# Performance work log

Hardware: AMD Instinct MI355X
Metric: run time of the kernel (lower is better)

The kernel has to match this reference:

```python
import jax, jax.numpy as jnp
import numpy as np

N_NODES = 20000
N_EDGES = 640000
IN_F = 128
CL1_F = 128
CL2_F = 128
OUT_F = 2


def setup_inputs() -> dict:
    key = jax.random.key(0)
    ks = jax.random.split(key, 8)
    x = jax.random.normal(ks[0], (N_NODES, IN_F), dtype=jnp.float32)
    edge_index = jax.random.randint(ks[1], (2, N_EDGES), 0, N_NODES, dtype=jnp.int64)
    s1 = 1.0 / np.sqrt(IN_F)
    s2 = 1.0 / np.sqrt(CL1_F)
    s3 = 1.0 / np.sqrt(CL2_F)
    W1 = jax.random.uniform(ks[2], (IN_F, CL1_F), jnp.float32, -s1, s1)
    b1 = jax.random.uniform(ks[3], (CL1_F,), jnp.float32, -s1, s1)
    W2 = jax.random.uniform(ks[4], (CL1_F, CL2_F), jnp.float32, -s2, s2)
    b2 = jax.random.uniform(ks[5], (CL2_F,), jnp.float32, -s2, s2)
    W3 = jax.random.uniform(ks[6], (CL2_F, OUT_F), jnp.float32, -s3, s3)
    b3 = jax.random.uniform(ks[7], (OUT_F,), jnp.float32, -s3, s3)
    return {"x": x, "edge_index": edge_index, "W1": W1, "b1": b1,
            "W2": W2, "b2": b2, "W3": W3, "b3": b3}


def _scatter_mean(feat_src, src, dst, n_nodes):
    # out[i] = mean over edges e with dst[e]==i of feat_src gathered at src[e]
    msg = feat_src[src]                                   # [E, F] gather
    summed = jax.ops.segment_sum(msg, dst, num_segments=n_nodes)  # [N, F]
    ones = jnp.ones((src.shape[0],), dtype=feat_src.dtype)
    cnt = jax.ops.segment_sum(ones, dst, num_segments=n_nodes)    # [N]
    return summed / jnp.maximum(cnt, 1.0)[:, None]


def _mpnn_layer(x, src, dst, W, b, n_nodes):
    aggr = _scatter_mean(x, src, dst, n_nodes)
    return jax.nn.relu(aggr @ W + b)


def reference(x, edge_index, W1, b1, W2, b2, W3, b3):
    src, dst = edge_index[0], edge_index[1]
    n = x.shape[0]
    h = _mpnn_layer(x, src, dst, W1, b1, n)   # conv1 (update relu); extra relu is no-op
    h = _mpnn_layer(h, src, dst, W2, b2, n)   # conv2
    # dropout in eval mode is identity
    return h @ W3 + b3
```

## Files before the change

### kernel.cpp

```cpp
#include <hip/hip_runtime.h>

#define N_NODES 20000
#define N_EDGES 640000
#define F 128
#define CAP 128


__global__ __launch_bounds__(256)
void bucket_kernel(const int* __restrict__ src, const int* __restrict__ dst,
                   int* __restrict__ cnt, int* __restrict__ bucket) {
    int e = blockIdx.x * blockDim.x + threadIdx.x;
    if (e >= N_EDGES) return;
    int d = dst[e];
    int pos = atomicAdd(&cnt[d], 1);
    if (pos < CAP) bucket[(size_t)d * CAP + pos] = src[e];
}

__global__ __launch_bounds__(256)
void gemm_kernel(const float* __restrict__ A, const float* __restrict__ W,
                 float* __restrict__ C) {
    __shared__ float As[32][F + 4];
    int tid  = threadIdx.x;
    int row0 = blockIdx.x * 32;

    const float4* A4 = (const float4*)(A + (size_t)row0 * F);
    for (int i = tid; i < 32 * 32; i += 256) {
        float4 v = A4[i];
        int r = i >> 5, c4 = (i & 31) * 4;
        *(float4*)&As[r][c4] = v;
    }
    __syncthreads();

    int tx = tid & 31, ty = tid >> 5;
    int c0 = tx * 4, r0 = ty * 4;
    float acc[4][4] = {};

    for (int k = 0; k < F; k += 4) {
        float4 a4[4];
#pragma unroll
        for (int i = 0; i < 4; ++i) a4[i] = *(const float4*)&As[r0 + i][k];
#pragma unroll
        for (int u = 0; u < 4; ++u) {
            float4 w = *(const float4*)(W + (size_t)(k + u) * F + c0);
#pragma unroll
            for (int i = 0; i < 4; ++i) {
                float a = (u == 0) ? a4[i].x : (u == 1) ? a4[i].y : (u == 2) ? a4[i].z : a4[i].w;
                acc[i][0] += a * w.x;
                acc[i][1] += a * w.y;
                acc[i][2] += a * w.z;
                acc[i][3] += a * w.w;
            }
        }
    }

#pragma unroll
    for (int i = 0; i < 4; ++i) {
        float4 o;
        o.x = acc[i][0]; o.y = acc[i][1]; o.z = acc[i][2]; o.w = acc[i][3];
        *(float4*)(C + (size_t)(row0 + r0 + i) * F + c0) = o;
    }
}

__global__ __launch_bounds__(256)
void agg_bias_relu_kernel(const float* __restrict__ y, const int* __restrict__ cnt,
                          const int* __restrict__ bucket, const float* __restrict__ b,
                          float* __restrict__ out) {
    int wid  = (blockIdx.x * blockDim.x + threadIdx.x) >> 6;
    int lane = threadIdx.x & 63;
    if (wid >= N_NODES) return;
    int half = lane >> 5;
    int sub  = lane & 31;
    int deg  = cnt[wid];
    const int* lst = bucket + (size_t)wid * CAP;
    const float4* f4 = (const float4*)y;

    float4 acc; acc.x = acc.y = acc.z = acc.w = 0.f;
    int j = 0;
    for (; j + 16 <= deg; j += 16) {
        int4 ia = *(const int4*)(lst + j);
        int4 ib = *(const int4*)(lst + j + 4);
        int4 ic = *(const int4*)(lst + j + 8);
        int4 id = *(const int4*)(lst + j + 12);
        int i0 = half ? ia.y : ia.x;
        int i1 = half ? ia.w : ia.z;
        int i2 = half ? ib.y : ib.x;
        int i3 = half ? ib.w : ib.z;
        int i4 = half ? ic.y : ic.x;
        int i5 = half ? ic.w : ic.z;
        int i6 = half ? id.y : id.x;
        int i7 = half ? id.w : id.z;
        float4 v0 = f4[(size_t)i0 * 32 + sub];
        float4 v1 = f4[(size_t)i1 * 32 + sub];
        float4 v2 = f4[(size_t)i2 * 32 + sub];
        float4 v3 = f4[(size_t)i3 * 32 + sub];
        float4 v4 = f4[(size_t)i4 * 32 + sub];
        float4 v5 = f4[(size_t)i5 * 32 + sub];
        float4 v6 = f4[(size_t)i6 * 32 + sub];
        float4 v7 = f4[(size_t)i7 * 32 + sub];
        acc.x += ((v0.x + v1.x) + (v2.x + v3.x)) + ((v4.x + v5.x) + (v6.x + v7.x));
        acc.y += ((v0.y + v1.y) + (v2.y + v3.y)) + ((v4.y + v5.y) + (v6.y + v7.y));
        acc.z += ((v0.z + v1.z) + (v2.z + v3.z)) + ((v4.z + v5.z) + (v6.z + v7.z));
        acc.w += ((v0.w + v1.w) + (v2.w + v3.w)) + ((v4.w + v5.w) + (v6.w + v7.w));
    }
    for (; j + 2 <= deg; j += 2) {
        int2 ii = *(const int2*)(lst + j);
        int idx = half ? ii.y : ii.x;
        float4 v = f4[(size_t)idx * 32 + sub];
        acc.x += v.x; acc.y += v.y; acc.z += v.z; acc.w += v.w;
    }
    if (j < deg && half == 0) {
        float4 v = f4[(size_t)lst[j] * 32 + sub];
        acc.x += v.x; acc.y += v.y; acc.z += v.z; acc.w += v.w;
    }
    acc.x += __shfl(acc.x, lane ^ 32);
    acc.y += __shfl(acc.y, lane ^ 32);
    acc.z += __shfl(acc.z, lane ^ 32);
    acc.w += __shfl(acc.w, lane ^ 32);

    if (half == 0) {
        float inv = 1.0f / fmaxf((float)deg, 1.0f);
        float4 bv = ((const float4*)b)[sub];
        float4 o;
        o.x = fmaxf(acc.x * inv + bv.x, 0.f);
        o.y = fmaxf(acc.y * inv + bv.y, 0.f);
        o.z = fmaxf(acc.z * inv + bv.z, 0.f);
        o.w = fmaxf(acc.w * inv + bv.w, 0.f);
        ((float4*)out)[(size_t)wid * 32 + sub] = o;
    }
}

__global__ __launch_bounds__(256)
void agg_final_kernel(const float* __restrict__ y, const int* __restrict__ cnt,
                      const int* __restrict__ bucket, const float* __restrict__ b,
                      const float* __restrict__ W3, const float* __restrict__ b3,
                      float* __restrict__ out) {
    int wid  = (blockIdx.x * blockDim.x + threadIdx.x) >> 6;
    int lane = threadIdx.x & 63;
    if (wid >= N_NODES) return;
    int half = lane >> 5;
    int sub  = lane & 31;
    int deg  = cnt[wid];
    const int* lst = bucket + (size_t)wid * CAP;
    const float4* f4 = (const float4*)y;

    float4 acc; acc.x = acc.y = acc.z = acc.w = 0.f;
    int j = 0;
    for (; j + 16 <= deg; j += 16) {
        int4 ia = *(const int4*)(lst + j);
        int4 ib = *(const int4*)(lst + j + 4);
        int4 ic = *(const int4*)(lst + j + 8);
        int4 id = *(const int4*)(lst + j + 12);
        int i0 = half ? ia.y : ia.x;
        int i1 = half ? ia.w : ia.z;
        int i2 = half ? ib.y : ib.x;
        int i3 = half ? ib.w : ib.z;
        int i4 = half ? ic.y : ic.x;
        int i5 = half ? ic.w : ic.z;
        int i6 = half ? id.y : id.x;
        int i7 = half ? id.w : id.z;
        float4 v0 = f4[(size_t)i0 * 32 + sub];
        float4 v1 = f4[(size_t)i1 * 32 + sub];
        float4 v2 = f4[(size_t)i2 * 32 + sub];
        float4 v3 = f4[(size_t)i3 * 32 + sub];
        float4 v4 = f4[(size_t)i4 * 32 + sub];
        float4 v5 = f4[(size_t)i5 * 32 + sub];
        float4 v6 = f4[(size_t)i6 * 32 + sub];
        float4 v7 = f4[(size_t)i7 * 32 + sub];
        acc.x += ((v0.x + v1.x) + (v2.x + v3.x)) + ((v4.x + v5.x) + (v6.x + v7.x));
        acc.y += ((v0.y + v1.y) + (v2.y + v3.y)) + ((v4.y + v5.y) + (v6.y + v7.y));
        acc.z += ((v0.z + v1.z) + (v2.z + v3.z)) + ((v4.z + v5.z) + (v6.z + v7.z));
        acc.w += ((v0.w + v1.w) + (v2.w + v3.w)) + ((v4.w + v5.w) + (v6.w + v7.w));
    }
    for (; j + 2 <= deg; j += 2) {
        int2 ii = *(const int2*)(lst + j);
        int idx = half ? ii.y : ii.x;
        float4 v = f4[(size_t)idx * 32 + sub];
        acc.x += v.x; acc.y += v.y; acc.z += v.z; acc.w += v.w;
    }
    if (j < deg && half == 0) {
        float4 v = f4[(size_t)lst[j] * 32 + sub];
        acc.x += v.x; acc.y += v.y; acc.z += v.z; acc.w += v.w;
    }
    acc.x += __shfl(acc.x, lane ^ 32);
    acc.y += __shfl(acc.y, lane ^ 32);
    acc.z += __shfl(acc.z, lane ^ 32);
    acc.w += __shfl(acc.w, lane ^ 32);

    float inv = 1.0f / fmaxf((float)deg, 1.0f);
    float4 bv = ((const float4*)b)[sub];
    float h0 = fmaxf(acc.x * inv + bv.x, 0.f);
    float h1 = fmaxf(acc.y * inv + bv.y, 0.f);
    float h2 = fmaxf(acc.z * inv + bv.z, 0.f);
    float h3 = fmaxf(acc.w * inv + bv.w, 0.f);
    float2 w0 = ((const float2*)W3)[sub * 4];
    float2 w1 = ((const float2*)W3)[sub * 4 + 1];
    float2 w2 = ((const float2*)W3)[sub * 4 + 2];
    float2 w3 = ((const float2*)W3)[sub * 4 + 3];
    float p0 = h0 * w0.x + h1 * w1.x + h2 * w2.x + h3 * w3.x;
    float p1 = h0 * w0.y + h1 * w1.y + h2 * w2.y + h3 * w3.y;
#pragma unroll
    for (int off = 16; off > 0; off >>= 1) {
        p0 += __shfl_down(p0, off, 32);
        p1 += __shfl_down(p1, off, 32);
    }
    if (lane == 0) {
        float2 o; o.x = p0 + b3[0]; o.y = p1 + b3[1];
        *(float2*)(out + (size_t)wid * 2) = o;
    }
}

extern "C" void kernel_launch(void* const* d_in, const int* in_sizes, int n_in,
                              void* d_out, int out_size, void* d_ws, size_t ws_size,
                              hipStream_t stream) {
    const float* x   = (const float*)d_in[0];
    const int*   ei  = (const int*)d_in[1];
    const int*   src = ei;
    const int*   dst = ei + N_EDGES;
    const float* W1 = (const float*)d_in[2];
    const float* b1 = (const float*)d_in[3];
    const float* W2 = (const float*)d_in[4];
    const float* b2 = (const float*)d_in[5];
    const float* W3 = (const float*)d_in[6];
    const float* b3 = (const float*)d_in[7];
    float* out = (float*)d_out;

    char* base = (char*)d_ws;
    size_t off = 0;
    auto take = [&](size_t bytes) -> char* {
        char* p = base + off;
        off += (bytes + 255) & ~(size_t)255;
        return p;
    };
    int*   cnt    = (int*)  take(N_NODES * sizeof(int));
    int*   bucket = (int*)  take((size_t)N_NODES * CAP * sizeof(int));
    float* y      = (float*)take((size_t)N_NODES * F * sizeof(float));
    float* h      = (float*)take((size_t)N_NODES * F * sizeof(float));

    hipMemsetAsync(cnt, 0, N_NODES * sizeof(int), stream);
    bucket_kernel<<<(N_EDGES + 255) / 256, 256, 0, stream>>>(src, dst, cnt, bucket);

    gemm_kernel<<<N_NODES / 32, 256, 0, stream>>>(x, W1, y);
    agg_bias_relu_kernel<<<(N_NODES * 64) / 256, 256, 0, stream>>>(y, cnt, bucket, b1, h);
    gemm_kernel<<<N_NODES / 32, 256, 0, stream>>>(h, W2, y);
    agg_final_kernel<<<(N_NODES * 64) / 256, 256, 0, stream>>>(y, cnt, bucket, b2, W3, b3, out);
}
```

Measured before the change: 215.2 us.

## Fuse edge bucketing into first GEMM launch and split aggregation across two waves

Merges the edge-bucketing kernel into the first GEMM launch by appending extra blocks that do the atomic bucket fill, so the two independent stages share one launch and can overlap. The aggregation kernels now give each node two waves that split the 16-neighbor chunks between them and combine their partial sums through shared memory. This doubles the parallelism per node to hide gather latency, at the cost of a block-wide barrier, shared-memory traffic, and half of the waves sitting idle during the epilogue.

```diff
diff --git a/kernel.cpp b/kernel.cpp
--- a/kernel.cpp
+++ b/kernel.cpp
@@ -4,25 +4,85 @@
 #define N_EDGES 640000
 #define F 128
 #define CAP 128
-
-
-__global__ __launch_bounds__(256)
-void bucket_kernel(const int* __restrict__ src, const int* __restrict__ dst,
-                   int* __restrict__ cnt, int* __restrict__ bucket) {
-    int e = blockIdx.x * blockDim.x + threadIdx.x;
-    if (e >= N_EDGES) return;
-    int d = dst[e];
-    int pos = atomicAdd(&cnt[d], 1);
-    if (pos < CAP) bucket[(size_t)d * CAP + pos] = src[e];
-}
-
-__global__ __launch_bounds__(256)
-void gemm_kernel(const float* __restrict__ A, const float* __restrict__ W,
-                 float* __restrict__ C) {
+#define GEMM_BLOCKS (N_NODES / 32)
+#define BUCKET_BLOCKS (N_EDGES / 256)
+
+
+__device__ __forceinline__ void gather16(const float4* __restrict__ f4,
+                                         const int* __restrict__ lst, int j,
+                                         int half, int sub, float4& acc) {
+    int4 ia = *(const int4*)(lst + j);
+    int4 ib = *(const int4*)(lst + j + 4);
+    int4 ic = *(const int4*)(lst + j + 8);
+    int4 id = *(const int4*)(lst + j + 12);
+    int i0 = half ? ia.y : ia.x;
+    int i1 = half ? ia.w : ia.z;
+    int i2 = half ? ib.y : ib.x;
+    int i3 = half ? ib.w : ib.z;
+    int i4 = half ? ic.y : ic.x;
+    int i5 = half ? ic.w : ic.z;
+    int i6 = half ? id.y : id.x;
+    int i7 = half ? id.w : id.z;
+    float4 v0 = f4[(size_t)i0 * 32 + sub];
+    float4 v1 = f4[(size_t)i1 * 32 + sub];
+    float4 v2 = f4[(size_t)i2 * 32 + sub];
+    float4 v3 = f4[(size_t)i3 * 32 + sub];
+    float4 v4 = f4[(size_t)i4 * 32 + sub];
+    float4 v5 = f4[(size_t)i5 * 32 + sub];
+    float4 v6 = f4[(size_t)i6 * 32 + sub];
+    float4 v7 = f4[(size_t)i7 * 32 + sub];
+    acc.x += ((v0.x + v1.x) + (v2.x + v3.x)) + ((v4.x + v5.x) + (v6.x + v7.x));
+    acc.y += ((v0.y + v1.y) + (v2.y + v3.y)) + ((v4.y + v5.y) + (v6.y + v7.y));
+    acc.z += ((v0.z + v1.z) + (v2.z + v3.z)) + ((v4.z + v5.z) + (v6.z + v7.z));
+    acc.w += ((v0.w + v1.w) + (v2.w + v3.w)) + ((v4.w + v5.w) + (v6.w + v7.w));
+}
+
+__device__ __forceinline__ float4 wave_gather(const float4* __restrict__ f4,
+                                              const int* __restrict__ lst, int deg,
+                                              int wh, int half, int sub, int lane) {
+    float4 acc; acc.x = acc.y = acc.z = acc.w = 0.f;
+    int nfull = deg >> 4;
+    for (int c = wh; c < nfull; c += 2)
+        gather16(f4, lst, c << 4, half, sub, acc);
+    if (wh == (nfull & 1)) {
+        int j = nfull << 4;
+        for (; j + 2 <= deg; j += 2) {
+            int2 ii = *(const int2*)(lst + j);
+            int idx = half ? ii.y : ii.x;
+            float4 v = f4[(size_t)idx * 32 + sub];
+            acc.x += v.x; acc.y += v.y; acc.z += v.z; acc.w += v.w;
+        }
+        if (j < deg && half == 0) {
+            float4 v = f4[(size_t)lst[j] * 32 + sub];
+            acc.x += v.x; acc.y += v.y; acc.z += v.z; acc.w += v.w;
+        }
+    }
+    acc.x += __shfl(acc.x, lane ^ 32);
+    acc.y += __shfl(acc.y, lane ^ 32);
+    acc.z += __shfl(acc.z, lane ^ 32);
+    acc.w += __shfl(acc.w, lane ^ 32);
+    return acc;
+}
+
+__global__ __launch_bounds__(256)
+void gemm_bucket_kernel(const float* __restrict__ A, const float* __restrict__ W,
+                        float* __restrict__ C,
+                        const int* __restrict__ src, const int* __restrict__ dst,
+                        int* __restrict__ cnt, int* __restrict__ bucket) {
     __shared__ float As[32][F + 4];
-    int tid  = threadIdx.x;
+    int tid = threadIdx.x;
+
+    if (blockIdx.x >= GEMM_BLOCKS) {
+        int e = (blockIdx.x - GEMM_BLOCKS) * 256 + tid;
+        if (e < N_EDGES) {
+            int d = dst[e];
+            int pos = atomicAdd(&cnt[d], 1);
+            if (pos < CAP) bucket[(size_t)d * CAP + pos] = src[e];
+        }
+        return;
+    }
+
     int row0 = blockIdx.x * 32;
-
     const float4* A4 = (const float4*)(A + (size_t)row0 * F);
     for (int i = tid; i < 32 * 32; i += 256) {
         float4 v = A4[i];
@@ -62,70 +122,79 @@
 }
 
 __global__ __launch_bounds__(256)
+void gemm_kernel(const float* __restrict__ A, const float* __restrict__ W,
+                 float* __restrict__ C) {
+    __shared__ float As[32][F + 4];
+    int tid  = threadIdx.x;
+    int row0 = blockIdx.x * 32;
+
+    const float4* A4 = (const float4*)(A + (size_t)row0 * F);
+    for (int i = tid; i < 32 * 32; i += 256) {
+        float4 v = A4[i];
+        int r = i >> 5, c4 = (i & 31) * 4;
+        *(float4*)&As[r][c4] = v;
+    }
+    __syncthreads();
+
+    int tx = tid & 31, ty = tid >> 5;
+    int c0 = tx * 4, r0 = ty * 4;
+    float acc[4][4] = {};
+
+    for (int k = 0; k < F; k += 4) {
+        float4 a4[4];
+#pragma unroll
+        for (int i = 0; i < 4; ++i) a4[i] = *(const float4*)&As[r0 + i][k];
+#pragma unroll
+        for (int u = 0; u < 4; ++u) {
+            float4 w = *(const float4*)(W + (size_t)(k + u) * F + c0);
+#pragma unroll
+            for (int i = 0; i < 4; ++i) {
+                float a = (u == 0) ? a4[i].x : (u == 1) ? a4[i].y : (u == 2) ? a4[i].z : a4[i].w;
+                acc[i][0] += a * w.x;
+                acc[i][1] += a * w.y;
+                acc[i][2] += a * w.z;
+                acc[i][3] += a * w.w;
+            }
+        }
+    }
+
+#pragma unroll
+    for (int i = 0; i < 4; ++i) {
+        float4 o;
+        o.x = acc[i][0]; o.y = acc[i][1]; o.z = acc[i][2]; o.w = acc[i][3];
+        *(float4*)(C + (size_t)(row0 + r0 + i) * F + c0) = o;
+    }
+}
+
+__global__ __launch_bounds__(256)
 void agg_bias_relu_kernel(const float* __restrict__ y, const int* __restrict__ cnt,
                           const int* __restrict__ bucket, const float* __restrict__ b,
                           float* __restrict__ out) {
-    int wid  = (blockIdx.x * blockDim.x + threadIdx.x) >> 6;
-    int lane = threadIdx.x & 63;
-    if (wid >= N_NODES) return;
-    int half = lane >> 5;
-    int sub  = lane & 31;
-    int deg  = cnt[wid];
-    const int* lst = bucket + (size_t)wid * CAP;
+    __shared__ float4 part[2][32];
+    int tid  = threadIdx.x;
+    int wave = tid >> 6, lane = tid & 63;
+    int nl   = wave >> 1;
+    int wh   = wave & 1;
+    int node = blockIdx.x * 2 + nl;
+    int half = lane >> 5, sub = lane & 31;
+    int deg  = cnt[node];
+    const int* lst = bucket + (size_t)node * CAP;
     const float4* f4 = (const float4*)y;
 
-    float4 acc; acc.x = acc.y = acc.z = acc.w = 0.f;
-    int j = 0;
-    for (; j + 16 <= deg; j += 16) {
-        int4 ia = *(const int4*)(lst + j);
-        int4 ib = *(const int4*)(lst + j + 4);
-        int4 ic = *(const int4*)(lst + j + 8);
-        int4 id = *(const int4*)(lst + j + 12);
-        int i0 = half ? ia.y : ia.x;
-        int i1 = half ? ia.w : ia.z;
-        int i2 = half ? ib.y : ib.x;
-        int i3 = half ? ib.w : ib.z;
-        int i4 = half ? ic.y : ic.x;
-        int i5 = half ? ic.w : ic.z;
-        int i6 = half ? id.y : id.x;
-        int i7 = half ? id.w : id.z;
-        float4 v0 = f4[(size_t)i0 * 32 + sub];
-        float4 v1 = f4[(size_t)i1 * 32 + sub];
-        float4 v2 = f4[(size_t)i2 * 32 + sub];
-        float4 v3 = f4[(size_t)i3 * 32 + sub];
-        float4 v4 = f4[(size_t)i4 * 32 + sub];
-        float4 v5 = f4[(size_t)i5 * 32 + sub];
-        float4 v6 = f4[(size_t)i6 * 32 + sub];
-        float4 v7 = f4[(size_t)i7 * 32 + sub];
-        acc.x += ((v0.x + v1.x) + (v2.x + v3.x)) + ((v4.x + v5.x) + (v6.x + v7.x));
-        acc.y += ((v0.y + v1.y) + (v2.y + v3.y)) + ((v4.y + v5.y) + (v6.y + v7.y));
-        acc.z += ((v0.z + v1.z) + (v2.z + v3.z)) + ((v4.z + v5.z) + (v6.z + v7.z));
-        acc.w += ((v0.w + v1.w) + (v2.w + v3.w)) + ((v4.w + v5.w) + (v6.w + v7.w));
-    }
-    for (; j + 2 <= deg; j += 2) {
-        int2 ii = *(const int2*)(lst + j);
-        int idx = half ? ii.y : ii.x;
-        float4 v = f4[(size_t)idx * 32 + sub];
-        acc.x += v.x; acc.y += v.y; acc.z += v.z; acc.w += v.w;
-    }
-    if (j < deg && half == 0) {
-        float4 v = f4[(size_t)lst[j] * 32 + sub];
-        acc.x += v.x; acc.y += v.y; acc.z += v.z; acc.w += v.w;
-    }
-    acc.x += __shfl(acc.x, lane ^ 32);
-    acc.y += __shfl(acc.y, lane ^ 32);
-    acc.z += __shfl(acc.z, lane ^ 32);
-    acc.w += __shfl(acc.w, lane ^ 32);
-
-    if (half == 0) {
+    float4 acc = wave_gather(f4, lst, deg, wh, half, sub, lane);
+
+    if (wh == 1 && half == 0) part[nl][sub] = acc;
+    __syncthreads();
+    if (wh == 0 && half == 0) {
+        float4 p = part[nl][sub];
         float inv = 1.0f / fmaxf((float)deg, 1.0f);
         float4 bv = ((const float4*)b)[sub];
         float4 o;
-        o.x = fmaxf(acc.x * inv + bv.x, 0.f);
-        o.y = fmaxf(acc.y * inv + bv.y, 0.f);
-        o.z = fmaxf(acc.z * inv + bv.z, 0.f);
-        o.w = fmaxf(acc.w * inv + bv.w, 0.f);
-        ((float4*)out)[(size_t)wid * 32 + sub] = o;
+        o.x = fmaxf((acc.x + p.x) * inv + bv.x, 0.f);
+        o.y = fmaxf((acc.y + p.y) * inv + bv.y, 0.f);
+        o.z = fmaxf((acc.z + p.z) * inv + bv.z, 0.f);
+        o.w = fmaxf((acc.w + p.w) * inv + bv.w, 0.f);
+        ((float4*)out)[(size_t)node * 32 + sub] = o;
     }
 }
 
@@ -134,78 +203,44 @@
                       const int* __restrict__ bucket, const float* __restrict__ b,
                       const float* __restrict__ W3, const float* __restrict__ b3,
                       float* __restrict__ out) {
-    int wid  = (blockIdx.x * blockDim.x + threadIdx.x) >> 6;
-    int lane = threadIdx.x & 63;
-    if (wid >= N_NODES) return;
-    int half = lane >> 5;
-    int sub  = lane & 31;
-    int deg  = cnt[wid];
-    const int* lst = bucket + (size_t)wid * CAP;
+    __shared__ float4 part[2][32];
+    int tid  = threadIdx.x;
+    int wave = tid >> 6, lane = tid & 63;
+    int nl   = wave >> 1;
+    int wh   = wave & 1;
+    int node = blockIdx.x * 2 + nl;
+    int half = lane >> 5, sub = lane & 31;
+    int deg  = cnt[node];
+    const int* lst = bucket + (size_t)node * CAP;
     const float4* f4 = (const float4*)y;
 
-    float4 acc; acc.x = acc.y = acc.z = acc.w = 0.f;
-    int j = 0;
-    for (; j + 16 <= deg; j += 16) {
-        int4 ia = *(const int4*)(lst + j);
-        int4 ib = *(const int4*)(lst + j + 4);
-        int4 ic = *(const int4*)(lst + j + 8);
-        int4 id = *(const int4*)(lst + j + 12);
-        int i0 = half ? ia.y : ia.x;
-        int i1 = half ? ia.w : ia.z;
-        int i2 = half ? ib.y : ib.x;
-        int i3 = half ? ib.w : ib.z;
-        int i4 = half ? ic.y : ic.x;
-        int i5 = half ? ic.w : ic.z;
-        int i6 = half ? id.y : id.x;
-        int i7 = half ? id.w : id.z;
-        float4 v0 = f4[(size_t)i0 * 32 + sub];
-        float4 v1 = f4[(size_t)i1 * 32 + sub];
-        float4 v2 = f4[(size_t)i2 * 32 + sub];
-        float4 v3 = f4[(size_t)i3 * 32 + sub];
-        float4 v4 = f4[(size_t)i4 * 32 + sub];
-        float4 v5 = f4[(size_t)i5 * 32 + sub];
-        float4 v6 = f4[(size_t)i6 * 32 + sub];
-        float4 v7 = f4[(size_t)i7 * 32 + sub];
-        acc.x += ((v0.x + v1.x) + (v2.x + v3.x)) + ((v4.x + v5.x) + (v6.x + v7.x));
-        acc.y += ((v0.y + v1.y) + (v2.y + v3.y)) + ((v4.y + v5.y) + (v6.y + v7.y));
-        acc.z += ((v0.z + v1.z) + (v2.z + v3.z)) + ((v4.z + v5.z) + (v6.z + v7.z));
-        acc.w += ((v0.w + v1.w) + (v2.w + v3.w)) + ((v4.w + v5.w) + (v6.w + v7.w));
-    }
-    for (; j + 2 <= deg; j += 2) {
-        int2 ii = *(const int2*)(lst + j);
-        int idx = half ? ii.y : ii.x;
-        float4 v = f4[(size_t)idx * 32 + sub];
-        acc.x += v.x; acc.y += v.y; acc.z += v.z; acc.w += v.w;
-    }
-    if (j < deg && half == 0) {
-        float4 v = f4[(size_t)lst[j] * 32 + sub];
-        acc.x += v.x; acc.y += v.y; acc.z += v.z; acc.w += v.w;
-    }
-    acc.x += __shfl(acc.x, lane ^ 32);
-    acc.y += __shfl(acc.y, lane ^ 32);
-    acc.z += __shfl(acc.z, lane ^ 32);
-    acc.w += __shfl(acc.w, lane ^ 32);
-
-    float inv = 1.0f / fmaxf((float)deg, 1.0f);
-    float4 bv = ((const float4*)b)[sub];
-    float h0 = fmaxf(acc.x * inv + bv.x, 0.f);
-    float h1 = fmaxf(acc.y * inv + bv.y, 0.f);
-    float h2 = fmaxf(acc.z * inv + bv.z, 0.f);
-    float h3 = fmaxf(acc.w * inv + bv.w, 0.f);
-    float2 w0 = ((const float2*)W3)[sub * 4];
-    float2 w1 = ((const float2*)W3)[sub * 4 + 1];
-    float2 w2 = ((const float2*)W3)[sub * 4 + 2];
-    float2 w3 = ((const float2*)W3)[sub * 4 + 3];
-    float p0 = h0 * w0.x + h1 * w1.x + h2 * w2.x + h3 * w3.x;
-    float p1 = h0 * w0.y + h1 * w1.y + h2 * w2.y + h3 * w3.y;
-#pragma unroll
-    for (int off = 16; off > 0; off >>= 1) {
-        p0 += __shfl_down(p0, off, 32);
-        p1 += __shfl_down(p1, off, 32);
-    }
-    if (lane == 0) {
-        float2 o; o.x = p0 + b3[0]; o.y = p1 + b3[1];
-        *(float2*)(out + (size_t)wid * 2) = o;
+    float4 acc = wave_gather(f4, lst, deg, wh, half, sub, lane);
+
+    if (wh == 1 && half == 0) part[nl][sub] = acc;
+    __syncthreads();
+    if (wh == 0 && half == 0) {
+        float4 p = part[nl][sub];
+        float inv = 1.0f / fmaxf((float)deg, 1.0f);
+        float4 bv = ((const float4*)b)[sub];
+        float h0 = fmaxf((acc.x + p.x) * inv + bv.x, 0.f);
+        float h1 = fmaxf((acc.y + p.y) * inv + bv.y, 0.f);
+        float h2 = fmaxf((acc.z + p.z) * inv + bv.z, 0.f);
+        float h3 = fmaxf((acc.w + p.w) * inv + bv.w, 0.f);
+        float2 w0 = ((const float2*)W3)[sub * 4];
+        float2 w1 = ((const float2*)W3)[sub * 4 + 1];
+        float2 w2 = ((const float2*)W3)[sub * 4 + 2];
+        float2 w3 = ((const float2*)W3)[sub * 4 + 3];
+        float p0 = h0 * w0.x + h1 * w1.x + h2 * w2.x + h3 * w3.x;
+        float p1 = h0 * w0.y + h1 * w1.y + h2 * w2.y + h3 * w3.y;
+#pragma unroll
+        for (int off = 16; off > 0; off >>= 1) {
+            p0 += __shfl_down(p0, off, 32);
+            p1 += __shfl_down(p1, off, 32);
+        }
+        if (sub == 0) {
+            float2 o; o.x = p0 + b3[0]; o.y = p1 + b3[1];
+            *(float2*)(out + (size_t)node * 2) = o;
+        }
     }
 }
 
@@ -237,10 +272,10 @@
     float* h      = (float*)take((size_t)N_NODES * F * sizeof(float));
 
     hipMemsetAsync(cnt, 0, N_NODES * sizeof(int), stream);
-    bucket_kernel<<<(N_EDGES + 255) / 256, 256, 0, stream>>>(src, dst, cnt, bucket);
-
-    gemm_kernel<<<N_NODES / 32, 256, 0, stream>>>(x, W1, y);
-    agg_bias_relu_kernel<<<(N_NODES * 64) / 256, 256, 0, stream>>>(y, cnt, bucket, b1, h);
+
+    gemm_bucket_kernel<<<GEMM_BLOCKS + BUCKET_BLOCKS, 256, 0, stream>>>(
+        x, W1, y, src, dst, cnt, bucket);
+    agg_bias_relu_kernel<<<N_NODES / 2, 256, 0, stream>>>(y, cnt, bucket, b1, h);
     gemm_kernel<<<N_NODES / 32, 256, 0, stream>>>(h, W2, y);
-    agg_final_kernel<<<(N_NODES * 64) / 256, 256, 0, stream>>>(y, cnt, bucket, b2, W3, b3, out);
-}
+    agg_final_kernel<<<N_NODES / 2, 256, 0, stream>>>(y, cnt, bucket, b2, W3, b3, out);
+}
```

New measurement: 213.0 us. Within noise of the previous version (-1.0%).
